# Kernel optimization log

Hardware: AMD Instinct MI355X
Metric: run time of the kernel (lower is better)

## Reference

```python
import jax, jax.numpy as jnp
import numpy as np

V, D, H, HID, L, C, R, ALPHA = 32000, 768, 12, 3072, 2, 2, 8, 16
B, S = 64, 512
HD = D // H
SCALE = ALPHA / R

def _lin(x, W, b, A, Bm):
    # LoRA linear (eval mode, dropout=identity): x @ W^T + b + scaling * (x @ A^T) @ B^T
    return x @ W.T + b + (x @ A.T) @ Bm.T * SCALE

def _ln(x, g, b):
    m = x.mean(-1, keepdims=True)
    v = ((x - m) ** 2).mean(-1, keepdims=True)
    return (x - m) / jnp.sqrt(v + 1e-5) * g + b

def setup_inputs():
    ks = iter(jax.random.split(jax.random.key(0), 64))
    def nrm(shape):
        return jax.random.normal(next(ks), shape, dtype=jnp.float32) * 0.02
    inp = {"tokens": jax.random.randint(next(ks), (B, S), 0, V)}
    inp["emb_W"] = nrm((V, D)); inp["emb_A"] = nrm((R, V)); inp["emb_B"] = nrm((D, R))
    dims = {"q": (D, D), "k": (D, D), "v": (D, D), "o": (D, D), "1": (D, HID), "2": (HID, D)}
    for nm, (di, do) in dims.items():
        inp["W" + nm] = nrm((L, do, di)); inp["b" + nm] = jnp.zeros((L, do), jnp.float32)
        inp["A" + nm] = nrm((L, R, di)); inp["B" + nm] = nrm((L, do, R))
    inp["g1"] = jnp.ones((L, D), jnp.float32); inp["be1"] = jnp.zeros((L, D), jnp.float32)
    inp["g2"] = jnp.ones((L, D), jnp.float32); inp["be2"] = jnp.zeros((L, D), jnp.float32)
    inp["fcW"] = nrm((C, D)); inp["fcb"] = jnp.zeros((C,), jnp.float32)
    inp["fcA"] = nrm((R, D)); inp["fcB"] = nrm((C, R))
    return inp

def reference(tokens, emb_W, emb_A, emb_B,
              Wq, bq, Aq, Bq, Wk, bk, Ak, Bk, Wv, bv, Av, Bv, Wo, bo, Ao, Bo,
              W1, b1, A1, B1, W2, b2, A2, B2,
              g1, be1, g2, be2, fcW, fcb, fcA, fcB):
    # LoRA embedding: W[tok] + scaling * A^T[tok] @ B^T
    x = emb_W[tokens] + (emb_A.T[tokens] @ emb_B.T) * SCALE      # (B, S, D)
    x = jnp.transpose(x, (1, 0, 2))                              # (S, B, D)
    for l in range(L):
        Q = _lin(x, Wq[l], bq[l], Aq[l], Bq[l]).reshape(S, B, H, HD).transpose(0, 2, 1, 3)
        K = _lin(x, Wk[l], bk[l], Ak[l], Bk[l]).reshape(S, B, H, HD).transpose(0, 2, 1, 3)
        Vt = _lin(x, Wv[l], bv[l], Av[l], Bv[l]).reshape(S, B, H, HD).transpose(0, 2, 1, 3)
        # Faithful to the source: attention mixes over the BATCH axis (S, H, B, B)
        scores = jnp.einsum('shbd,shcd->shbc', Q, K) / jnp.sqrt(jnp.float32(HD))
        probs = jax.nn.softmax(scores, axis=-1)
        ao = jnp.einsum('shbc,shcd->shbd', probs, Vt).transpose(0, 2, 1, 3).reshape(S, B, D)
        ao = _lin(ao, Wo[l], bo[l], Ao[l], Bo[l])
        x = _ln(x + ao, g1[l], be1[l])
        ff = _lin(jax.nn.relu(_lin(x, W1[l], b1[l], A1[l], B1[l])), W2[l], b2[l], A2[l], B2[l])
        x = _ln(x + ff, g2[l], be2[l])
    return _lin(x.mean(0), fcW, fcb, fcA, fcB)                   # (B, C)
```

## Files before the change

### kernel.cpp

```cpp
#include <hip/hip_runtime.h>
#include <hip/hip_bf16.h>

#define VSZ   32000
#define DSZ   768
#define HN    12
#define HIDSZ 3072
#define NL    2
#define CN    2
#define RR    8
#define SCALEF 2.0f
#define BBATCH 64
#define SSEQ  512
#define HDIM  64
#define NTOK  (BBATCH*SSEQ)
#define QKVM  (3*DSZ)

typedef __attribute__((ext_vector_type(8))) short bf16x8;
typedef __attribute__((ext_vector_type(4))) float floatx4;

__device__ __forceinline__ unsigned short f2bf_raw(float f) {
    __hip_bfloat16 h = __float2bfloat16(f);
    return __builtin_bit_cast(unsigned short, h);
}
__device__ __forceinline__ float bf2f(__hip_bfloat16 h) {
    return __bfloat162float(h);
}

__device__ __forceinline__ void gload16(const void* g, void* l) {
    __builtin_amdgcn_global_load_lds(
        (const __attribute__((address_space(1))) unsigned int*)g,
        (__attribute__((address_space(3))) unsigned int*)l, 16, 0, 0);
}

__global__ __launch_bounds__(256) void embed_kernel(
    const int* __restrict__ tokens, const float* __restrict__ embW,
    const float* __restrict__ embA, const float* __restrict__ embB,
    __hip_bfloat16* __restrict__ xb)
{
    int n = blockIdx.x;
    int s = n / BBATCH, b = n % BBATCH;
    int tok = tokens[b * SSEQ + s];
    __shared__ float a[RR];
    if (threadIdx.x < RR) a[threadIdx.x] = embA[(size_t)threadIdx.x * VSZ + tok];
    __syncthreads();
    for (int d = threadIdx.x; d < DSZ; d += 256) {
        float val = embW[(size_t)tok * DSZ + d];
        float lo = 0.f;
        #pragma unroll
        for (int r = 0; r < RR; ++r) lo += a[r] * embB[d * RR + r];
        xb[(size_t)n * DSZ + d] = __float2bfloat16(val + SCALEF * lo);
    }
}

__global__ __launch_bounds__(256) void weff_kernel(
    const float* __restrict__ W, const float* __restrict__ A,
    const float* __restrict__ Bm, __hip_bfloat16* __restrict__ Weff, int K)
{
    int i = blockIdx.x * 256 + threadIdx.x;
    int o = blockIdx.y;
    float acc = W[(size_t)o * K + i];
    #pragma unroll
    for (int r = 0; r < RR; ++r)
        acc += SCALEF * Bm[o * RR + r] * A[(size_t)r * K + i];
    Weff[(size_t)o * K + i] = __float2bfloat16(acc);
}

__global__ __launch_bounds__(256) void biascat_kernel(
    const float* __restrict__ b0, const float* __restrict__ b1v,
    const float* __restrict__ b2v, float* __restrict__ out)
{
    int t = blockIdx.y * 256 + threadIdx.x;
    const float* src = (blockIdx.x == 0) ? b0 : (blockIdx.x == 1) ? b1v : b2v;
    out[blockIdx.x * DSZ + t] = src[t];
}

#define BM2  256
#define BK2  64
#define ABUF (BM2*BK2)

__device__ __forceinline__ void stage_half(
    const unsigned short* __restrict__ g, unsigned short* l,
    int h, int ld, int k0, int t, int sk)
{
    #pragma unroll
    for (int it = 0; it < 2; ++it) {
        int rl = it * 64 + (t >> 3);
        gload16(g + (size_t)(h * 128 + rl) * ld + k0 + sk,
                l + (size_t)(h * 1024 + it * 512 + t) * 8);
    }
}

__device__ __forceinline__ void ph_enter() {
    __builtin_amdgcn_sched_barrier(0);
    __builtin_amdgcn_s_barrier();
    asm volatile("s_waitcnt lgkmcnt(0)" ::: "memory");
    __builtin_amdgcn_sched_barrier(0);
    __builtin_amdgcn_s_setprio(1);
}

__device__ __forceinline__ void ph_exit() {
    __builtin_amdgcn_s_setprio(0);
    __builtin_amdgcn_sched_barrier(0);
    __builtin_amdgcn_s_barrier();
    __builtin_amdgcn_sched_barrier(0);
}

template<bool RELU, bool ADDRES>
__global__ __launch_bounds__(512, 2) void mgemm256_kernel(
    const __hip_bfloat16* __restrict__ X, const __hip_bfloat16* __restrict__ W,
    const float* __restrict__ bias, const __hip_bfloat16* __restrict__ res,
    __hip_bfloat16* __restrict__ Y, int K, int ldx, int ldy)
{
    __shared__ __align__(16) unsigned short As[2 * ABUF];
    __shared__ __align__(16) unsigned short Bs[2 * ABUF];

    const int t    = threadIdx.x;
    const int wv   = t >> 6;
    const int lane = t & 63;
    const int fm   = lane & 15;
    const int fq   = lane >> 4;
    const int wm   = wv >> 2;
    const int wn   = wv & 3;

    const int nbx = gridDim.x;
    int lin = blockIdx.y * nbx + blockIdx.x;
    {
        const int nwg = nbx * gridDim.y;
        int q = nwg >> 3, r = nwg & 7;
        int xcd = lin & 7, idx = lin >> 3;
        lin = (xcd < r ? xcd * (q + 1) : r * (q + 1) + (xcd - r) * q) + idx;
    }
    const int bm = lin % nbx;
    const int bn = lin / nbx;

    const unsigned short* Xg = (const unsigned short*)X + (size_t)bm * 256 * ldx;
    const unsigned short* Wg = (const unsigned short*)W + (size_t)bn * 256 * K;
    const int sk = ((t & 7) ^ ((t >> 3) & 7)) * 8;
    const int nt = K / BK2;

    floatx4 acc[2][2][4][2];
    #pragma unroll
    for (int a = 0; a < 2; ++a)
        #pragma unroll
        for (int b = 0; b < 2; ++b)
            #pragma unroll
            for (int c = 0; c < 4; ++c)
                #pragma unroll
                for (int d = 0; d < 2; ++d)
                    acc[a][b][c][d] = (floatx4){0.f, 0.f, 0.f, 0.f};

    const int swzg = (fq ^ (fm & 7)) * 8;
    int aoff[4], boff[2];
    #pragma unroll
    for (int mf = 0; mf < 4; ++mf) aoff[mf] = (wm * 64 + mf * 16 + fm) * 64 + swzg;
    #pragma unroll
    for (int nf = 0; nf < 2; ++nf) boff[nf] = (wn * 32 + nf * 16 + fm) * 64 + swzg;

    stage_half(Xg, As, 0, ldx, 0, t, sk);
    stage_half(Wg, Bs, 0, K,   0, t, sk);
    stage_half(Xg, As, 1, ldx, 0, t, sk);
    stage_half(Wg, Bs, 1, K,   0, t, sk);
    if (nt > 1) {
        stage_half(Xg, As + ABUF, 0, ldx, BK2, t, sk);
        stage_half(Wg, Bs + ABUF, 0, K,   BK2, t, sk);
        stage_half(Wg, Bs + ABUF, 1, K,   BK2, t, sk);
        asm volatile("s_waitcnt vmcnt(6)" ::: "memory");
    } else {
        asm volatile("s_waitcnt vmcnt(0)" ::: "memory");
    }
    __builtin_amdgcn_sched_barrier(0);
    __builtin_amdgcn_s_barrier();
    __builtin_amdgcn_sched_barrier(0);

    for (int kt = 0; kt < nt; ++kt) {
        const unsigned short* Ab = As + (kt & 1) * ABUF;
        const unsigned short* Bb = Bs + (kt & 1) * ABUF;
        unsigned short* Aoth  = As + ((kt & 1) ^ 1) * ABUF;
        unsigned short* Asame = (unsigned short*)Ab;
        unsigned short* Bsame = (unsigned short*)Bb;
        const int k1 = (kt + 1) * BK2;
        const int k2 = (kt + 2) * BK2;
        bf16x8 af[4][2], bf0[2][2], bf1[2][2];

        #pragma unroll
        for (int mf = 0; mf < 4; ++mf) {
            af[mf][0] = *(const bf16x8*)&Ab[aoff[mf]];
            af[mf][1] = *(const bf16x8*)&Ab[aoff[mf] ^ 32];
        }
        #pragma unroll
        for (int nf = 0; nf < 2; ++nf) {
            bf0[nf][0] = *(const bf16x8*)&Bb[boff[nf]];
            bf0[nf][1] = *(const bf16x8*)&Bb[boff[nf] ^ 32];
        }
        if (kt + 1 < nt) stage_half(Xg, Aoth, 1, ldx, k1, t, sk);
        ph_enter();
        #pragma unroll
        for (int mf = 0; mf < 4; ++mf)
            #pragma unroll
            for (int nf = 0; nf < 2; ++nf) {
                acc[0][0][mf][nf] = __builtin_amdgcn_mfma_f32_16x16x32_bf16(
                    af[mf][0], bf0[nf][0], acc[0][0][mf][nf], 0, 0, 0);
                acc[0][0][mf][nf] = __builtin_amdgcn_mfma_f32_16x16x32_bf16(
                    af[mf][1], bf0[nf][1], acc[0][0][mf][nf], 0, 0, 0);
            }
        ph_exit();

        #pragma unroll
        for (int nf = 0; nf < 2; ++nf) {
            bf1[nf][0] = *(const bf16x8*)&Bb[(boff[nf] + 8192)];
            bf1[nf][1] = *(const bf16x8*)&Bb[(boff[nf] + 8192) ^ 32];
        }
        if (kt + 2 < nt) stage_half(Xg, Asame, 0, ldx, k2, t, sk);
        ph_enter();
        #pragma unroll
        for (int mf = 0; mf < 4; ++mf)
            #pragma unroll
            for (int nf = 0; nf < 2; ++nf) {
                acc[0][1][mf][nf] = __builtin_amdgcn_mfma_f32_16x16x32_bf16(
                    af[mf][0], bf1[nf][0], acc[0][1][mf][nf], 0, 0, 0);
                acc[0][1][mf][nf] = __builtin_amdgcn_mfma_f32_16x16x32_bf16(
                    af[mf][1], bf1[nf][1], acc[0][1][mf][nf], 0, 0, 0);
            }
        ph_exit();

        #pragma unroll
        for (int mf = 0; mf < 4; ++mf) {
            af[mf][0] = *(const bf16x8*)&Ab[(aoff[mf] + 8192)];
            af[mf][1] = *(const bf16x8*)&Ab[(aoff[mf] + 8192) ^ 32];
        }
        if (kt + 2 < nt) stage_half(Wg, Bsame, 0, K, k2, t, sk);
        ph_enter();
        #pragma unroll
        for (int mf = 0; mf < 4; ++mf)
            #pragma unroll
            for (int nf = 0; nf < 2; ++nf) {
                acc[1][0][mf][nf] = __builtin_amdgcn_mfma_f32_16x16x32_bf16(
                    af[mf][0], bf0[nf][0], acc[1][0][mf][nf], 0, 0, 0);
                acc[1][0][mf][nf] = __builtin_amdgcn_mfma_f32_16x16x32_bf16(
                    af[mf][1], bf0[nf][1], acc[1][0][mf][nf], 0, 0, 0);
            }
        ph_exit();

        if (kt + 2 < nt) stage_half(Wg, Bsame, 1, K, k2, t, sk);
        ph_enter();
        #pragma unroll
        for (int mf = 0; mf < 4; ++mf)
            #pragma unroll
            for (int nf = 0; nf < 2; ++nf) {
                acc[1][1][mf][nf] = __builtin_amdgcn_mfma_f32_16x16x32_bf16(
                    af[mf][0], bf1[nf][0], acc[1][1][mf][nf], 0, 0, 0);
                acc[1][1][mf][nf] = __builtin_amdgcn_mfma_f32_16x16x32_bf16(
                    af[mf][1], bf1[nf][1], acc[1][1][mf][nf], 0, 0, 0);
            }
        __builtin_amdgcn_s_setprio(0);
        __builtin_amdgcn_sched_barrier(0);
        if (kt + 2 < nt) {
            asm volatile("s_waitcnt vmcnt(6)" ::: "memory");
        } else if (kt + 1 < nt) {
            asm volatile("s_waitcnt vmcnt(0)" ::: "memory");
        }
        __builtin_amdgcn_sched_barrier(0);
        __builtin_amdgcn_s_barrier();
        __builtin_amdgcn_sched_barrier(0);
    }

    #pragma unroll
    for (int mh = 0; mh < 2; ++mh)
        #pragma unroll
        for (int nh = 0; nh < 2; ++nh)
            #pragma unroll
            for (int nf = 0; nf < 2; ++nf) {
                const int col = bn * 256 + nh * 128 + wn * 32 + nf * 16 + fm;
                const float bj = bias[col];
                #pragma unroll
                for (int mf = 0; mf < 4; ++mf) {
                    const int row0 = bm * 256 + mh * 128 + wm * 64 + mf * 16 + fq * 4;
                    #pragma unroll
                    for (int r = 0; r < 4; ++r) {
                        float v = acc[mh][nh][mf][nf][r] + bj;
                        if (RELU) v = fmaxf(v, 0.f);
                        size_t off = (size_t)(row0 + r) * ldy + col;
                        if (ADDRES) v += bf2f(res[off]);
                        Y[off] = __float2bfloat16(v);
                    }
                }
            }
}

__global__ __launch_bounds__(256) void attn_kernel(
    const __hip_bfloat16* __restrict__ qkvb, __hip_bfloat16* __restrict__ aob)
{
    __shared__ __align__(16) unsigned short Vt[64][72];
    __shared__ __align__(16) unsigned short Ps[4][16][72];
    const int t    = threadIdx.x;
    const int wv   = t >> 6;
    const int lane = t & 63;
    const int fm   = lane & 15;
    const int fq   = lane >> 4;
    const int sp   = blockIdx.x / HN;
    const int h    = blockIdx.x % HN;
    const unsigned short* qg =
        (const unsigned short*)qkvb + (size_t)sp * BBATCH * QKVM + h * HDIM;

    {
        const int c = lane, d0 = wv * 16;
        const unsigned short* vrow = qg + 2 * DSZ + (size_t)c * QKVM + d0;
        bf16x8 v0 = *(const bf16x8*)vrow;
        bf16x8 v1 = *(const bf16x8*)(vrow + 8);
        #pragma unroll
        for (int i = 0; i < 8; ++i) {
            Vt[d0 + i][c]     = (unsigned short)v0[i];
            Vt[d0 + 8 + i][c] = (unsigned short)v1[i];
        }
    }

    const unsigned short* qrow = qg + (size_t)(wv * 16 + fm) * QKVM + fq * 8;
    bf16x8 af0 = *(const bf16x8*)qrow;
    bf16x8 af1 = *(const bf16x8*)(qrow + 32);
    bf16x8 bk0[4], bk1[4];
    #pragma unroll
    for (int jt = 0; jt < 4; ++jt) {
        const unsigned short* krow = qg + DSZ + (size_t)(jt * 16 + fm) * QKVM + fq * 8;
        bk0[jt] = *(const bf16x8*)krow;
        bk1[jt] = *(const bf16x8*)(krow + 32);
    }

    floatx4 sc[4];
    #pragma unroll
    for (int jt = 0; jt < 4; ++jt) sc[jt] = (floatx4){0.f, 0.f, 0.f, 0.f};
    #pragma unroll
    for (int jt = 0; jt < 4; ++jt) {
        sc[jt] = __builtin_amdgcn_mfma_f32_16x16x32_bf16(af0, bk0[jt], sc[jt], 0, 0, 0);
        sc[jt] = __builtin_amdgcn_mfma_f32_16x16x32_bf16(af1, bk1[jt], sc[jt], 0, 0, 0);
    }
    #pragma unroll
    for (int jt = 0; jt < 4; ++jt)
        #pragma unroll
        for (int r = 0; r < 4; ++r) sc[jt][r] *= 0.125f;

    float pr[4][4];
    #pragma unroll
    for (int r = 0; r < 4; ++r) {
        float m = fmaxf(fmaxf(sc[0][r], sc[1][r]), fmaxf(sc[2][r], sc[3][r]));
        #pragma unroll
        for (int msk = 1; msk < 16; msk <<= 1) m = fmaxf(m, __shfl_xor(m, msk, 64));
        float s = 0.f;
        #pragma unroll
        for (int jt = 0; jt < 4; ++jt) { pr[jt][r] = __expf(sc[jt][r] - m); s += pr[jt][r]; }
        #pragma unroll
        for (int msk = 1; msk < 16; msk <<= 1) s += __shfl_xor(s, msk, 64);
        float inv = 1.f / s;
        #pragma unroll
        for (int jt = 0; jt < 4; ++jt) pr[jt][r] *= inv;
    }

    #pragma unroll
    for (int jt = 0; jt < 4; ++jt)
        #pragma unroll
        for (int r = 0; r < 4; ++r)
            Ps[wv][fq * 4 + r][jt * 16 + fm] = f2bf_raw(pr[jt][r]);

    __syncthreads();

    bf16x8 ap0 = *(const bf16x8*)&Ps[wv][fm][fq * 8];
    bf16x8 ap1 = *(const bf16x8*)&Ps[wv][fm][32 + fq * 8];
    floatx4 ov[4];
    #pragma unroll
    for (int jt = 0; jt < 4; ++jt) ov[jt] = (floatx4){0.f, 0.f, 0.f, 0.f};
    #pragma unroll
    for (int jt = 0; jt < 4; ++jt) {
        bf16x8 bv0 = *(const bf16x8*)&Vt[jt * 16 + fm][fq * 8];
        bf16x8 bv1 = *(const bf16x8*)&Vt[jt * 16 + fm][32 + fq * 8];
        ov[jt] = __builtin_amdgcn_mfma_f32_16x16x32_bf16(ap0, bv0, ov[jt], 0, 0, 0);
        ov[jt] = __builtin_amdgcn_mfma_f32_16x16x32_bf16(ap1, bv1, ov[jt], 0, 0, 0);
    }

    __hip_bfloat16* obase = aob + ((size_t)sp * BBATCH + wv * 16 + fq * 4) * DSZ + h * HDIM;
    #pragma unroll
    for (int jt = 0; jt < 4; ++jt)
        #pragma unroll
        for (int r = 0; r < 4; ++r)
            obase[(size_t)r * DSZ + jt * 16 + fm] = __float2bfloat16(ov[jt][r]);
}

__device__ __forceinline__ float block_sum256(float vsum, volatile float* red) {
    #pragma unroll
    for (int off = 32; off > 0; off >>= 1) vsum += __shfl_down(vsum, off, 64);
    if ((threadIdx.x & 63) == 0) red[threadIdx.x >> 6] = vsum;
    __syncthreads();
    return red[0] + red[1] + red[2] + red[3];
}

__global__ __launch_bounds__(256) void ln_kernel(
    const __hip_bfloat16* __restrict__ src, __hip_bfloat16* __restrict__ dst,
    const float* __restrict__ g, const float* __restrict__ be)
{
    __shared__ float red1[4];
    __shared__ float red2[4];
    const int n = blockIdx.x;
    const int t = threadIdx.x;
    const __hip_bfloat16* row = src + (size_t)n * DSZ;
    __hip_bfloat16* orow = dst + (size_t)n * DSZ;
    float v0 = bf2f(row[t]), v1 = bf2f(row[t + 256]), v2 = bf2f(row[t + 512]);
    float total = block_sum256(v0 + v1 + v2, red1);
    float mean = total * (1.0f / DSZ);
    float d0 = v0 - mean, d1 = v1 - mean, d2 = v2 - mean;
    __syncthreads();
    float var = block_sum256(d0 * d0 + d1 * d1 + d2 * d2, red2) * (1.0f / DSZ);
    float rstd = rsqrtf(var + 1e-5f);
    orow[t]       = __float2bfloat16(d0 * rstd * g[t]       + be[t]);
    orow[t + 256] = __float2bfloat16(d1 * rstd * g[t + 256] + be[t + 256]);
    orow[t + 512] = __float2bfloat16(d2 * rstd * g[t + 512] + be[t + 512]);
}

__global__ __launch_bounds__(256) void meanS_kernel(
    const __hip_bfloat16* __restrict__ x, float* __restrict__ xm)
{
    int idx = blockIdx.x * 256 + threadIdx.x;
    int b = idx / DSZ, d = idx % DSZ;
    float acc = 0.f;
    for (int s = 0; s < SSEQ; ++s)
        acc += bf2f(x[((size_t)s * BBATCH + b) * DSZ + d]);
    xm[idx] = acc * (1.0f / SSEQ);
}

__global__ __launch_bounds__(128) void fc_kernel(
    const float* __restrict__ xm, const float* __restrict__ fcW,
    const float* __restrict__ fcb, const float* __restrict__ fcA,
    const float* __restrict__ fcBm, float* __restrict__ out)
{
    int t = threadIdx.x;
    if (t >= BBATCH * CN) return;
    int b = t / CN, c = t % CN;
    float acc = fcb[c];
    float lora[RR];
    #pragma unroll
    for (int r = 0; r < RR; ++r) lora[r] = 0.f;
    for (int d = 0; d < DSZ; ++d) {
        float xv = xm[b * DSZ + d];
        acc += xv * fcW[c * DSZ + d];
        #pragma unroll
        for (int r = 0; r < RR; ++r) lora[r] += xv * fcA[r * DSZ + d];
    }
    float lo = 0.f;
    #pragma unroll
    for (int r = 0; r < RR; ++r) lo += lora[r] * fcBm[c * RR + r];
    out[b * CN + c] = acc + SCALEF * lo;
}

extern "C" void kernel_launch(void* const* d_in, const int* in_sizes, int n_in,
                              void* d_out, int out_size, void* d_ws, size_t ws_size,
                              hipStream_t stream) {
    const int*   tokens = (const int*)  d_in[0];
    const float* embW   = (const float*)d_in[1];
    const float* embA   = (const float*)d_in[2];
    const float* embB   = (const float*)d_in[3];
    const float* Wq = (const float*)d_in[4],  *bq = (const float*)d_in[5],
               * Aq = (const float*)d_in[6],  *Bq = (const float*)d_in[7];
    const float* Wk = (const float*)d_in[8],  *bk = (const float*)d_in[9],
               * Ak = (const float*)d_in[10], *Bk = (const float*)d_in[11];
    const float* Wv = (const float*)d_in[12], *bv = (const float*)d_in[13],
               * Av = (const float*)d_in[14], *Bv = (const float*)d_in[15];
    const float* Wo = (const float*)d_in[16], *bo = (const float*)d_in[17],
               * Ao = (const float*)d_in[18], *Bo = (const float*)d_in[19];
    const float* W1 = (const float*)d_in[20], *b1 = (const float*)d_in[21],
               * A1 = (const float*)d_in[22], *B1 = (const float*)d_in[23];
    const float* W2 = (const float*)d_in[24], *b2 = (const float*)d_in[25],
               * A2 = (const float*)d_in[26], *B2 = (const float*)d_in[27];
    const float* g1 = (const float*)d_in[28], *be1 = (const float*)d_in[29];
    const float* g2 = (const float*)d_in[30], *be2 = (const float*)d_in[31];
    const float* fcW = (const float*)d_in[32], *fcb = (const float*)d_in[33];
    const float* fcA = (const float*)d_in[34], *fcBm = (const float*)d_in[35];

    const size_t ND = (size_t)NTOK * DSZ;

    const size_t X_F    = ND / 2;
    const size_t XT_F   = ND / 2;
    const size_t WQKV_F = (size_t)QKVM * DSZ / 2;
    const size_t WO_F   = (size_t)DSZ * DSZ / 2;
    const size_t WF1_F  = (size_t)HIDSZ * DSZ / 2;
    const size_t WF2_F  = (size_t)DSZ * HIDSZ / 2;
    const size_t BQKV_F = 2304;
    const size_t XM_F   = (size_t)BBATCH * DSZ;
    const size_t fixedF = X_F + XT_F + WQKV_F + WO_F + WF1_F + WF2_F + BQKV_F + XM_F;
    const size_t availF = ws_size / 4;

    int schunk = 2;
    const int cand[6] = {512, 256, 128, 64, 32, 16};
    for (int i = 0; i < 6; ++i) {
        size_t chunkF = (size_t)cand[i] * BBATCH * (HIDSZ / 2);
        if (fixedF + chunkF <= availF) { schunk = cand[i]; break; }
    }
    const int Nc = schunk * BBATCH;
    const int nchunk = SSEQ / schunk;

    float* p = (float*)d_ws;
    __hip_bfloat16* x  = (__hip_bfloat16*)p;     p += X_F;
    __hip_bfloat16* xt = (__hip_bfloat16*)p;     p += XT_F;
    __hip_bfloat16* wqkvb = (__hip_bfloat16*)p;  p += WQKV_F;
    __hip_bfloat16* wob   = (__hip_bfloat16*)p;  p += WO_F;
    __hip_bfloat16* wf1b  = (__hip_bfloat16*)p;  p += WF1_F;
    __hip_bfloat16* wf2b  = (__hip_bfloat16*)p;  p += WF2_F;
    float* bqkv = p;                             p += BQKV_F;
    float* xm   = p;                             p += XM_F;
    __hip_bfloat16* cb16 = (__hip_bfloat16*)p;
    __hip_bfloat16* qkvb = cb16;
    __hip_bfloat16* aob  = cb16 + (size_t)Nc * QKVM;
    __hip_bfloat16* hb   = cb16;

    embed_kernel<<<NTOK, 256, 0, stream>>>(tokens, embW, embA, embB, x);

    for (int l = 0; l < NL; ++l) {
        const size_t oDD = (size_t)l * DSZ * DSZ;
        const size_t oDH = (size_t)l * HIDSZ * DSZ;
        const size_t oRD = (size_t)l * RR * DSZ;
        const size_t oRH = (size_t)l * RR * HIDSZ;
        const size_t oDR = (size_t)l * DSZ * RR;
        const size_t oHR = (size_t)l * HIDSZ * RR;

        weff_kernel<<<dim3(3, DSZ), 256, 0, stream>>>(Wq + oDD, Aq + oRD, Bq + oDR, wqkvb, DSZ);
        weff_kernel<<<dim3(3, DSZ), 256, 0, stream>>>(Wk + oDD, Ak + oRD, Bk + oDR, wqkvb + (size_t)DSZ * DSZ, DSZ);
        weff_kernel<<<dim3(3, DSZ), 256, 0, stream>>>(Wv + oDD, Av + oRD, Bv + oDR, wqkvb + (size_t)2 * DSZ * DSZ, DSZ);
        biascat_kernel<<<dim3(3, 3), 256, 0, stream>>>(bq + (size_t)l * DSZ, bk + (size_t)l * DSZ, bv + (size_t)l * DSZ, bqkv);
        weff_kernel<<<dim3(3, DSZ), 256, 0, stream>>>(Wo + oDD, Ao + oRD, Bo + oDR, wob, DSZ);
        weff_kernel<<<dim3(3, HIDSZ), 256, 0, stream>>>(W1 + oDH, A1 + oRD, B1 + oHR, wf1b, DSZ);
        weff_kernel<<<dim3(12, DSZ), 256, 0, stream>>>(W2 + oDH, A2 + oRH, B2 + oDR, wf2b, HIDSZ);

        const float* bo_l = bo + (size_t)l * DSZ;
        const float* b1_l = b1 + (size_t)l * HIDSZ;
        const float* b2_l = b2 + (size_t)l * DSZ;

        for (int c = 0; c < nchunk; ++c) {
            __hip_bfloat16* xc  = x  + (size_t)c * Nc * DSZ;
            __hip_bfloat16* xtc = xt + (size_t)c * Nc * DSZ;

            mgemm256_kernel<false, false><<<dim3(Nc / BM2, QKVM / BM2), 512, 0, stream>>>(
                xc, wqkvb, bqkv, nullptr, qkvb, DSZ, DSZ, QKVM);

            attn_kernel<<<schunk * HN, 256, 0, stream>>>(qkvb, aob);

            mgemm256_kernel<false, true><<<dim3(Nc / BM2, DSZ / BM2), 512, 0, stream>>>(
                aob, wob, bo_l, xc, xtc, DSZ, DSZ, DSZ);
            ln_kernel<<<Nc, 256, 0, stream>>>(xtc, xc, g1 + (size_t)l * DSZ, be1 + (size_t)l * DSZ);

            mgemm256_kernel<true, false><<<dim3(Nc / BM2, HIDSZ / BM2), 512, 0, stream>>>(
                xc, wf1b, b1_l, nullptr, hb, DSZ, DSZ, HIDSZ);

            mgemm256_kernel<false, true><<<dim3(Nc / BM2, DSZ / BM2), 512, 0, stream>>>(
                hb, wf2b, b2_l, xc, xtc, HIDSZ, HIDSZ, DSZ);
            ln_kernel<<<Nc, 256, 0, stream>>>(xtc, xc, g2 + (size_t)l * DSZ, be2 + (size_t)l * DSZ);
        }
    }

    meanS_kernel<<<(BBATCH * DSZ) / 256, 256, 0, stream>>>(x, xm);
    fc_kernel<<<1, 128, 0, stream>>>(xm, fcW, fcb, fcA, fcBm, (float*)d_out);
}
```

Baseline: 1.882 ms.

## Prefetch next tile's LDS fragments across phases and swap tile rasterization order

Restructures the 256x256 GEMM main loop so LDS fragment reads for the next phase (and the next k-tile's first fragments) are issued before the current MFMA phase. Partial lgkmcnt waits replace full drains, so ds_reads overlap with matrix math. It also changes block-to-tile mapping to iterate N-tiles fastest within each XCD chunk, aiming for better L2 reuse of X rows. The cost is higher register pressure from the double fragment sets and fragile hand-tuned vmcnt/lgkmcnt counts, which could cause races if miscounted.

```diff
diff --git a/kernel.cpp b/kernel.cpp
--- a/kernel.cpp
+++ b/kernel.cpp
@@ -78,6 +78,8 @@
 #define BK2  64
 #define ABUF (BM2*BK2)
 
+#define SB0() __builtin_amdgcn_sched_barrier(0)
+
 __device__ __forceinline__ void stage_half(
     const unsigned short* __restrict__ g, unsigned short* l,
     int h, int ld, int k0, int t, int sk)
@@ -90,19 +92,11 @@
     }
 }
 
-__device__ __forceinline__ void ph_enter() {
-    __builtin_amdgcn_sched_barrier(0);
-    __builtin_amdgcn_s_barrier();
-    asm volatile("s_waitcnt lgkmcnt(0)" ::: "memory");
-    __builtin_amdgcn_sched_barrier(0);
-    __builtin_amdgcn_s_setprio(1);
-}
-
 __device__ __forceinline__ void ph_exit() {
     __builtin_amdgcn_s_setprio(0);
-    __builtin_amdgcn_sched_barrier(0);
+    SB0();
     __builtin_amdgcn_s_barrier();
-    __builtin_amdgcn_sched_barrier(0);
+    SB0();
 }
 
 template<bool RELU, bool ADDRES>
@@ -123,15 +117,16 @@
     const int wn   = wv & 3;
 
     const int nbx = gridDim.x;
+    const int nby = gridDim.y;
     int lin = blockIdx.y * nbx + blockIdx.x;
     {
-        const int nwg = nbx * gridDim.y;
+        const int nwg = nbx * nby;
         int q = nwg >> 3, r = nwg & 7;
         int xcd = lin & 7, idx = lin >> 3;
         lin = (xcd < r ? xcd * (q + 1) : r * (q + 1) + (xcd - r) * q) + idx;
     }
-    const int bm = lin % nbx;
-    const int bn = lin / nbx;
+    const int bn = lin % nby;
+    const int bm = lin / nby;
 
     const unsigned short* Xg = (const unsigned short*)X + (size_t)bm * 256 * ldx;
     const unsigned short* Wg = (const unsigned short*)W + (size_t)bn * 256 * K;
@@ -168,100 +163,136 @@
     } else {
         asm volatile("s_waitcnt vmcnt(0)" ::: "memory");
     }
-    __builtin_amdgcn_sched_barrier(0);
+    SB0();
     __builtin_amdgcn_s_barrier();
-    __builtin_amdgcn_sched_barrier(0);
+    SB0();
+
+    bf16x8 af0[4][2], af1[4][2], bf0[2][2], bf1[2][2];
+    #pragma unroll
+    for (int mf = 0; mf < 4; ++mf) {
+        af0[mf][0] = *(const bf16x8*)&As[aoff[mf]];
+        af0[mf][1] = *(const bf16x8*)&As[aoff[mf] ^ 32];
+    }
+    #pragma unroll
+    for (int nf = 0; nf < 2; ++nf) {
+        bf0[nf][0] = *(const bf16x8*)&Bs[boff[nf]];
+        bf0[nf][1] = *(const bf16x8*)&Bs[boff[nf] ^ 32];
+    }
+    SB0();
 
     for (int kt = 0; kt < nt; ++kt) {
         const unsigned short* Ab = As + (kt & 1) * ABUF;
         const unsigned short* Bb = Bs + (kt & 1) * ABUF;
-        unsigned short* Aoth  = As + ((kt & 1) ^ 1) * ABUF;
+        unsigned short* AobW = As + ((kt & 1) ^ 1) * ABUF;
+        const unsigned short* AobR = AobW;
+        const unsigned short* BobR = Bs + ((kt & 1) ^ 1) * ABUF;
         unsigned short* Asame = (unsigned short*)Ab;
         unsigned short* Bsame = (unsigned short*)Bb;
         const int k1 = (kt + 1) * BK2;
         const int k2 = (kt + 2) * BK2;
-        bf16x8 af[4][2], bf0[2][2], bf1[2][2];
-
-        #pragma unroll
-        for (int mf = 0; mf < 4; ++mf) {
-            af[mf][0] = *(const bf16x8*)&Ab[aoff[mf]];
-            af[mf][1] = *(const bf16x8*)&Ab[aoff[mf] ^ 32];
-        }
-        #pragma unroll
-        for (int nf = 0; nf < 2; ++nf) {
-            bf0[nf][0] = *(const bf16x8*)&Bb[boff[nf]];
-            bf0[nf][1] = *(const bf16x8*)&Bb[boff[nf] ^ 32];
-        }
-        if (kt + 1 < nt) stage_half(Xg, Aoth, 1, ldx, k1, t, sk);
-        ph_enter();
-        #pragma unroll
-        for (int mf = 0; mf < 4; ++mf)
-            #pragma unroll
-            for (int nf = 0; nf < 2; ++nf) {
-                acc[0][0][mf][nf] = __builtin_amdgcn_mfma_f32_16x16x32_bf16(
-                    af[mf][0], bf0[nf][0], acc[0][0][mf][nf], 0, 0, 0);
-                acc[0][0][mf][nf] = __builtin_amdgcn_mfma_f32_16x16x32_bf16(
-                    af[mf][1], bf0[nf][1], acc[0][0][mf][nf], 0, 0, 0);
-            }
-        ph_exit();
 
         #pragma unroll
         for (int nf = 0; nf < 2; ++nf) {
             bf1[nf][0] = *(const bf16x8*)&Bb[(boff[nf] + 8192)];
             bf1[nf][1] = *(const bf16x8*)&Bb[(boff[nf] + 8192) ^ 32];
         }
+        SB0();
+        if (kt + 1 < nt) stage_half(Xg, AobW, 1, ldx, k1, t, sk);
+        SB0();
+        __builtin_amdgcn_s_barrier();
+        asm volatile("s_waitcnt lgkmcnt(4)" ::: "memory");
+        SB0();
+        __builtin_amdgcn_s_setprio(1);
+        #pragma unroll
+        for (int mf = 0; mf < 4; ++mf)
+            #pragma unroll
+            for (int nf = 0; nf < 2; ++nf) {
+                acc[0][0][mf][nf] = __builtin_amdgcn_mfma_f32_16x16x32_bf16(
+                    af0[mf][0], bf0[nf][0], acc[0][0][mf][nf], 0, 0, 0);
+                acc[0][0][mf][nf] = __builtin_amdgcn_mfma_f32_16x16x32_bf16(
+                    af0[mf][1], bf0[nf][1], acc[0][0][mf][nf], 0, 0, 0);
+            }
+        ph_exit();
+
+        #pragma unroll
+        for (int mf = 0; mf < 4; ++mf) {
+            af1[mf][0] = *(const bf16x8*)&Ab[(aoff[mf] + 8192)];
+            af1[mf][1] = *(const bf16x8*)&Ab[(aoff[mf] + 8192) ^ 32];
+        }
+        SB0();
         if (kt + 2 < nt) stage_half(Xg, Asame, 0, ldx, k2, t, sk);
-        ph_enter();
+        SB0();
+        __builtin_amdgcn_s_barrier();
+        asm volatile("s_waitcnt lgkmcnt(8)" ::: "memory");
+        SB0();
+        __builtin_amdgcn_s_setprio(1);
         #pragma unroll
         for (int mf = 0; mf < 4; ++mf)
             #pragma unroll
             for (int nf = 0; nf < 2; ++nf) {
                 acc[0][1][mf][nf] = __builtin_amdgcn_mfma_f32_16x16x32_bf16(
-                    af[mf][0], bf1[nf][0], acc[0][1][mf][nf], 0, 0, 0);
+                    af0[mf][0], bf1[nf][0], acc[0][1][mf][nf], 0, 0, 0);
                 acc[0][1][mf][nf] = __builtin_amdgcn_mfma_f32_16x16x32_bf16(
-                    af[mf][1], bf1[nf][1], acc[0][1][mf][nf], 0, 0, 0);
+                    af0[mf][1], bf1[nf][1], acc[0][1][mf][nf], 0, 0, 0);
             }
         ph_exit();
 
-        #pragma unroll
-        for (int mf = 0; mf < 4; ++mf) {
-            af[mf][0] = *(const bf16x8*)&Ab[(aoff[mf] + 8192)];
-            af[mf][1] = *(const bf16x8*)&Ab[(aoff[mf] + 8192) ^ 32];
-        }
         if (kt + 2 < nt) stage_half(Wg, Bsame, 0, K, k2, t, sk);
-        ph_enter();
+        SB0();
+        __builtin_amdgcn_s_barrier();
+        asm volatile("s_waitcnt lgkmcnt(0)" ::: "memory");
+        SB0();
+        __builtin_amdgcn_s_setprio(1);
         #pragma unroll
         for (int mf = 0; mf < 4; ++mf)
             #pragma unroll
             for (int nf = 0; nf < 2; ++nf) {
                 acc[1][0][mf][nf] = __builtin_amdgcn_mfma_f32_16x16x32_bf16(
-                    af[mf][0], bf0[nf][0], acc[1][0][mf][nf], 0, 0, 0);
+                    af1[mf][0], bf0[nf][0], acc[1][0][mf][nf], 0, 0, 0);
                 acc[1][0][mf][nf] = __builtin_amdgcn_mfma_f32_16x16x32_bf16(
-                    af[mf][1], bf0[nf][1], acc[1][0][mf][nf], 0, 0, 0);
+                    af1[mf][1], bf0[nf][1], acc[1][0][mf][nf], 0, 0, 0);
             }
         ph_exit();
 
+        asm volatile("s_waitcnt vmcnt(4)" ::: "memory");
+        SB0();
+        if (kt + 1 < nt) {
+            #pragma unroll
+            for (int mf = 0; mf < 4; ++mf) {
+                af0[mf][0] = *(const bf16x8*)&AobR[aoff[mf]];
+                af0[mf][1] = *(const bf16x8*)&AobR[aoff[mf] ^ 32];
+            }
+            #pragma unroll
+            for (int nf = 0; nf < 2; ++nf) {
+                bf0[nf][0] = *(const bf16x8*)&BobR[boff[nf]];
+                bf0[nf][1] = *(const bf16x8*)&BobR[boff[nf] ^ 32];
+            }
+        }
+        SB0();
         if (kt + 2 < nt) stage_half(Wg, Bsame, 1, K, k2, t, sk);
-        ph_enter();
+        SB0();
+        __builtin_amdgcn_s_barrier();
+        SB0();
+        __builtin_amdgcn_s_setprio(1);
         #pragma unroll
         for (int mf = 0; mf < 4; ++mf)
             #pragma unroll
             for (int nf = 0; nf < 2; ++nf) {
                 acc[1][1][mf][nf] = __builtin_amdgcn_mfma_f32_16x16x32_bf16(
-                    af[mf][0], bf1[nf][0], acc[1][1][mf][nf], 0, 0, 0);
+                    af1[mf][0], bf1[nf][0], acc[1][1][mf][nf], 0, 0, 0);
                 acc[1][1][mf][nf] = __builtin_amdgcn_mfma_f32_16x16x32_bf16(
-                    af[mf][1], bf1[nf][1], acc[1][1][mf][nf], 0, 0, 0);
+                    af1[mf][1], bf1[nf][1], acc[1][1][mf][nf], 0, 0, 0);
             }
         __builtin_amdgcn_s_setprio(0);
-        __builtin_amdgcn_sched_barrier(0);
+        SB0();
         if (kt + 2 < nt) {
             asm volatile("s_waitcnt vmcnt(6)" ::: "memory");
         } else if (kt + 1 < nt) {
             asm volatile("s_waitcnt vmcnt(0)" ::: "memory");
         }
-        __builtin_amdgcn_sched_barrier(0);
+        SB0();
         __builtin_amdgcn_s_barrier();
-        __builtin_amdgcn_sched_barrier(0);
+        SB0();
     }
 
     #pragma unroll
```

New measurement: 1.856 ms. No clear change (-1.4%).
